# Optimization experiments

Hardware: AMD Instinct MI355X
Metric: run time of the kernel (lower is better)

Reference implementation:

```python
import jax, jax.numpy as jnp
import numpy as np

N = 100000
F_IN = 128
HID = 8
HEADS = 8
CLASSES = 40
NEG_SLOPE = 0.2


def gat_conv(x, src, dst, W, a_src, a_dst, bias, heads, out_c):
    # x: [N, F]; W: [F, heads*out_c]; a_src/a_dst: [heads, out_c]; bias: [heads*out_c]
    n = x.shape[0]
    h = (x @ W).reshape(n, heads, out_c)                       # [N, H, C]
    al_src = jnp.sum(h * a_src, axis=-1)                       # [N, H]
    al_dst = jnp.sum(h * a_dst, axis=-1)                       # [N, H]
    e = jax.nn.leaky_relu(al_src[src] + al_dst[dst], NEG_SLOPE)  # [E, H]
    # segment softmax over destination node (PyG softmax over edge_index[1])
    m = jax.ops.segment_max(e, dst, num_segments=n)            # [N, H]
    m = jnp.where(jnp.isfinite(m), m, 0.0)
    ex = jnp.exp(e - m[dst])
    denom = jax.ops.segment_sum(ex, dst, num_segments=n)       # [N, H]
    alpha = ex / denom[dst]                                    # [E, H]
    msg = h[src] * alpha[:, :, None]                           # [E, H, C]
    out = jax.ops.segment_sum(msg, dst, num_segments=n)        # [N, H, C]
    return out.reshape(n, heads * out_c) + bias


def setup_inputs() -> dict:
    key = jax.random.key(0)
    ks = jax.random.split(key, 12)
    E = 1600000
    x = jax.random.normal(ks[0], (N, F_IN), dtype=jnp.float32)
    edge_index = jax.random.randint(ks[1], (2, E), 0, N, dtype=jnp.int32)
    # layer 1: in=F_IN, out=HID, heads=HEADS, concat -> 64 channels
    s1 = 1.0 / np.sqrt(F_IN)
    W1 = jax.random.uniform(ks[2], (F_IN, HEADS * HID), jnp.float32, -s1, s1)
    a_src1 = jax.random.uniform(ks[3], (HEADS, HID), jnp.float32, -0.3, 0.3)
    a_dst1 = jax.random.uniform(ks[4], (HEADS, HID), jnp.float32, -0.3, 0.3)
    b1 = jnp.zeros((HEADS * HID,), jnp.float32)
    # layer 2: in=64, out=CLASSES, heads=1
    d2 = HEADS * HID
    s2 = 1.0 / np.sqrt(d2)
    W2 = jax.random.uniform(ks[5], (d2, CLASSES), jnp.float32, -s2, s2)
    a_src2 = jax.random.uniform(ks[6], (1, CLASSES), jnp.float32, -0.3, 0.3)
    a_dst2 = jax.random.uniform(ks[7], (1, CLASSES), jnp.float32, -0.3, 0.3)
    b2 = jnp.zeros((CLASSES,), jnp.float32)
    return {"x": x, "edge_index": edge_index, "W1": W1, "a_src1": a_src1,
            "a_dst1": a_dst1, "b1": b1, "W2": W2, "a_src2": a_src2,
            "a_dst2": a_dst2, "b2": b2}


def reference(x, edge_index, W1, a_src1, a_dst1, b1, W2, a_src2, a_dst2, b2):
    # PyG GATConv adds self-loops by default
    loops = jnp.arange(N, dtype=edge_index.dtype)
    src = jnp.concatenate([edge_index[0], loops])
    dst = jnp.concatenate([edge_index[1], loops])
    h = gat_conv(x, src, dst, W1, a_src1, a_dst1, b1, HEADS, HID)
    h = jax.nn.relu(h)  # dropout is identity in eval mode
    out = gat_conv(h, src, dst, W2, a_src2, a_dst2, b2, 1, CLASSES)
    return jax.nn.log_softmax(out, axis=1)
```

## Files before the change

### kernel.cpp

```cpp
#include <hip/hip_runtime.h>
#include <hip/hip_bf16.h>
#include <math.h>

#define FIN 128
#define HID 8
#define HEADS 8
#define C1 64
#define CLS 40
#define NSLOPE 0.2f
#define NINF (-__builtin_inff())

typedef __hip_bfloat16 bf16;
typedef int vint4 __attribute__((ext_vector_type(4)));

__device__ __forceinline__ float lrelu(float x) { return x >= 0.f ? x : NSLOPE * x; }
__device__ __forceinline__ vint4 ldnt4(const int* p) {
    return __builtin_nontemporal_load((const vint4*)p);
}

__global__ __launch_bounds__(256) void k_deg(const int* __restrict__ ei, int E,
                                             int n, int* __restrict__ deg) {
    int g = blockIdx.x & 7;
    int per8 = (n + 7) >> 3;
    int lo = g * per8, hi = min(n, lo + per8);
    int idx = (blockIdx.x >> 3) * 256 + threadIdx.x;
    int e0 = idx * 4;
    if (e0 + 3 < E) {
        vint4 dv = ldnt4(ei + E + e0);
        if (dv.x >= lo && dv.x < hi) atomicAdd(&deg[dv.x], 1);
        if (dv.y >= lo && dv.y < hi) atomicAdd(&deg[dv.y], 1);
        if (dv.z >= lo && dv.z < hi) atomicAdd(&deg[dv.z], 1);
        if (dv.w >= lo && dv.w < hi) atomicAdd(&deg[dv.w], 1);
    } else {
        int e_end = min(e0 + 4, E);
        for (int e = e0; e < e_end; ++e) {
            int dd = ei[E + e];
            if (dd >= lo && dd < hi) atomicAdd(&deg[dd], 1);
        }
    }
}

__global__ __launch_bounds__(256) void k_scan1(const int* __restrict__ deg,
    int* __restrict__ rowstart, int* __restrict__ bsum, int n) {
    __shared__ int sm[256];
    int t = threadIdx.x, i = blockIdx.x * 256 + t;
    int v = (i < n) ? deg[i] + 1 : 0;
    sm[t] = v; __syncthreads();
    int x = v;
    for (int off = 1; off < 256; off <<= 1) {
        int tv = (t >= off) ? sm[t - off] : 0;
        __syncthreads();
        x += tv; sm[t] = x; __syncthreads();
    }
    if (i < n) rowstart[i] = x - v;
    if (t == 255) bsum[blockIdx.x] = x;
}

__global__ __launch_bounds__(512) void k_scan2(int* __restrict__ bsum, int nb) {
    __shared__ int sm[512];
    int t = threadIdx.x;
    int v = (t < nb) ? bsum[t] : 0;
    sm[t] = v; __syncthreads();
    int x = v;
    for (int off = 1; off < 512; off <<= 1) {
        int tv = (t >= off) ? sm[t - off] : 0;
        __syncthreads();
        x += tv; sm[t] = x; __syncthreads();
    }
    if (t < nb) bsum[t] = x - v;
}

__global__ void k_scan3(int* __restrict__ rowstart, const int* __restrict__ bsum,
                        int n, int total) {
    int i = blockIdx.x * blockDim.x + threadIdx.x;
    if (i < n) rowstart[i] += bsum[i >> 8];
    if (i == 0) rowstart[n] = total;
}

__global__ __launch_bounds__(256) void k_scatter(const int* __restrict__ ei,
    int E, int En, int n, int* __restrict__ rowcur, int* __restrict__ csr) {
    int g = blockIdx.x & 7;
    int per8 = (n + 7) >> 3;
    int lo = g * per8, hi = min(n, lo + per8);
    int idx = (blockIdx.x >> 3) * 256 + threadIdx.x;
    int e0 = idx * 4;
    if (e0 + 3 < E) {
        vint4 dv = ldnt4(ei + E + e0);
        vint4 sv = ldnt4(ei + e0);
        if (dv.x >= lo && dv.x < hi) csr[atomicAdd(&rowcur[dv.x], 1)] = sv.x;
        if (dv.y >= lo && dv.y < hi) csr[atomicAdd(&rowcur[dv.y], 1)] = sv.y;
        if (dv.z >= lo && dv.z < hi) csr[atomicAdd(&rowcur[dv.z], 1)] = sv.z;
        if (dv.w >= lo && dv.w < hi) csr[atomicAdd(&rowcur[dv.w], 1)] = sv.w;
    } else {
        int e_end = min(e0 + 4, En);
        for (int e = e0; e < e_end; ++e) {
            int s, d;
            if (e < E) { s = ei[e]; d = ei[E + e]; } else { s = d = e - E; }
            if (d >= lo && d < hi) csr[atomicAdd(&rowcur[d], 1)] = s;
        }
    }
}

__global__ __launch_bounds__(256) void gemm1_kernel(
    const float* __restrict__ x, const float* __restrict__ W1,
    const float* __restrict__ a_src, const float* __restrict__ a_dst,
    bf16* __restrict__ h1b, float* __restrict__ alS, float* __restrict__ alD, int n) {
    __shared__ float4 Wl[FIN][C1 / 4];
    __shared__ float xs[64][FIN + 4];
    int t = threadIdx.x;
    const float4* W4 = (const float4*)W1;
    for (int i = t; i < FIN * (C1 / 4); i += 256) Wl[i / (C1 / 4)][i % (C1 / 4)] = W4[i];
    int node0 = blockIdx.x * 64;
    for (int i = t; i < 64 * (FIN / 4); i += 256) {
        int r = i / (FIN / 4), c = i % (FIN / 4);
        int nn = node0 + r;
        float4 v = {0.f, 0.f, 0.f, 0.f};
        if (nn < n) v = ((const float4*)x)[(size_t)nn * (FIN / 4) + c];
        *(float4*)&xs[r][c * 4] = v;
    }
    __syncthreads();
    int cg = t & 15, ng = t >> 4;
    int head = cg >> 1, hc = (cg & 1) * 4;
    float acc[4][4];
    #pragma unroll
    for (int i = 0; i < 4; ++i)
        for (int j = 0; j < 4; ++j) acc[i][j] = 0.f;
    #pragma unroll 2
    for (int k = 0; k < FIN; ++k) {
        float4 w = Wl[k][cg];
        #pragma unroll
        for (int i = 0; i < 4; ++i) {
            float xv = xs[ng * 4 + i][k];
            acc[i][0] += xv * w.x; acc[i][1] += xv * w.y;
            acc[i][2] += xv * w.z; acc[i][3] += xv * w.w;
        }
    }
    float a_s[4], a_d[4];
    #pragma unroll
    for (int j = 0; j < 4; ++j) {
        a_s[j] = a_src[head * HID + hc + j];
        a_d[j] = a_dst[head * HID + hc + j];
    }
    #pragma unroll
    for (int i = 0; i < 4; ++i) {
        int node = node0 + ng * 4 + i;
        float as = acc[i][0] * a_s[0] + acc[i][1] * a_s[1]
                 + acc[i][2] * a_s[2] + acc[i][3] * a_s[3];
        float ad = acc[i][0] * a_d[0] + acc[i][1] * a_d[1]
                 + acc[i][2] * a_d[2] + acc[i][3] * a_d[3];
        as += __shfl_xor(as, 1, 64);
        ad += __shfl_xor(ad, 1, 64);
        if (node < n) {
            union { ushort4 u; bf16 b[4]; } pk;
            #pragma unroll
            for (int j = 0; j < 4; ++j) pk.b[j] = __float2bfloat16(acc[i][j]);
            ((ushort4*)h1b)[(size_t)node * (C1 / 4) + cg] = pk.u;
            if ((cg & 1) == 0) {
                alS[node * HEADS + head] = as;
                alD[node * HEADS + head] = ad;
            }
        }
    }
}

__global__ __launch_bounds__(256) void k_agg1(
    const int* __restrict__ csr, const int* __restrict__ rowend,
    const int* __restrict__ deg,
    const float* __restrict__ alS, const float* __restrict__ alD,
    const bf16* __restrict__ h1b, const float* __restrict__ b1,
    const float* __restrict__ W2, const float* __restrict__ aS2,
    const float* __restrict__ aD2,
    bf16* __restrict__ h2b, float* __restrict__ alS2, float* __restrict__ alD2,
    int n) {
    __shared__ int    ls[4][64];
    __shared__ float4 lp4[4][128];
    __shared__ float  xrow[4][64];
    __shared__ float  Wl[C1][CLS];
    int t = threadIdx.x;
    for (int i = t; i < C1 * CLS; i += 256) Wl[i / CLS][i % CLS] = W2[i];
    __syncthreads();
    int lane = t & 63, wv = t >> 6;
    int d = blockIdx.x * 4 + wv;
    if (d >= n) return;
    float4 ad0 = *(const float4*)(alD + d * HEADS);
    float4 ad1 = *(const float4*)(alD + d * HEADS + 4);
    float adh[8] = {ad0.x, ad0.y, ad0.z, ad0.w, ad1.x, ad1.y, ad1.z, ad1.w};
    int cnt  = deg[d] + 1;
    int base = rowend[d] - cnt;
    int hsel = lane >> 3;
    float acc = 0.f, den = 0.f;
    const float* lpf = (const float*)&lp4[wv][0];
    for (int jb = 0; jb < cnt; jb += 64) {
        int ec = min(64, cnt - jb);
        int jj = jb + lane;
        bool on = jj < cnt;
        int s = on ? csr[base + jj] : 0;
        ls[wv][lane] = s;
        float4 a0 = *(const float4*)(alS + s * HEADS);
        float4 a1 = *(const float4*)(alS + s * HEADS + 4);
        float av[8] = {a0.x, a0.y, a0.z, a0.w, a1.x, a1.y, a1.z, a1.w};
        float pv[8];
        #pragma unroll
        for (int h = 0; h < 8; ++h)
            pv[h] = on ? __expf(lrelu(av[h] + adh[h])) : 0.f;
        lp4[wv][lane * 2]     = make_float4(pv[0], pv[1], pv[2], pv[3]);
        lp4[wv][lane * 2 + 1] = make_float4(pv[4], pv[5], pv[6], pv[7]);
        int j = 0;
        for (; j + 4 <= ec; j += 4) {
            int s0 = ls[wv][j],     s1 = ls[wv][j + 1];
            int s2 = ls[wv][j + 2], s3 = ls[wv][j + 3];
            float p0 = lpf[(j    ) * 8 + hsel], p1 = lpf[(j + 1) * 8 + hsel];
            float p2 = lpf[(j + 2) * 8 + hsel], p3 = lpf[(j + 3) * 8 + hsel];
            float v0 = __bfloat162float(h1b[s0 * C1 + lane]);
            float v1 = __bfloat162float(h1b[s1 * C1 + lane]);
            float v2 = __bfloat162float(h1b[s2 * C1 + lane]);
            float v3 = __bfloat162float(h1b[s3 * C1 + lane]);
            acc = fmaf(p0, v0, acc); acc = fmaf(p1, v1, acc);
            acc = fmaf(p2, v2, acc); acc = fmaf(p3, v3, acc);
            den += p0 + p1 + p2 + p3;
        }
        for (; j < ec; ++j) {
            int s0 = ls[wv][j];
            float p0 = lpf[j * 8 + hsel];
            acc = fmaf(p0, __bfloat162float(h1b[s0 * C1 + lane]), acc);
            den += p0;
        }
    }
    float v = acc / den + b1[lane];
    v = v > 0.f ? v : 0.f;
    xrow[wv][lane] = v;
    bool act = lane < CLS;
    float h2c = 0.f;
    if (act) {
        #pragma unroll 8
        for (int k = 0; k < C1; ++k) h2c = fmaf(xrow[wv][k], Wl[k][lane], h2c);
    }
    float as2 = act ? h2c * aS2[lane] : 0.f;
    float ad2 = act ? h2c * aD2[lane] : 0.f;
    #pragma unroll
    for (int off = 1; off < 64; off <<= 1) {
        as2 += __shfl_xor(as2, off, 64);
        ad2 += __shfl_xor(ad2, off, 64);
    }
    if (act) h2b[d * CLS + lane] = __float2bfloat16(h2c);
    if (lane == 0) { alS2[d] = as2; alD2[d] = ad2; }
}

__global__ __launch_bounds__(256) void k_agg2(
    const int* __restrict__ csr, const int* __restrict__ rowend,
    const int* __restrict__ deg,
    const float* __restrict__ alS, const float* __restrict__ alD,
    const bf16* __restrict__ h2b, const float* __restrict__ b2,
    float* __restrict__ out, int n) {
    __shared__ int2 lsp[4][64];
    int lane = threadIdx.x & 63, wv = threadIdx.x >> 6;
    int d = blockIdx.x * 4 + wv;
    if (d >= n) return;
    float ad = alD[d];
    int cnt  = deg[d] + 1;
    int base = rowend[d] - cnt;
    bool act = lane < CLS;
    float acc = 0.f, den = 0.f;
    for (int jb = 0; jb < cnt; jb += 64) {
        int ec = min(64, cnt - jb);
        int jj = jb + lane;
        bool on = jj < cnt;
        int s = on ? csr[base + jj] : 0;
        float p = on ? __expf(lrelu(alS[s] + ad)) : 0.f;
        den += p;
        lsp[wv][lane] = make_int2(s, __float_as_int(p));
        if (act) {
            int j = 0;
            for (; j + 4 <= ec; j += 4) {
                int2 e0 = lsp[wv][j],     e1 = lsp[wv][j + 1];
                int2 e2 = lsp[wv][j + 2], e3 = lsp[wv][j + 3];
                float v0 = __bfloat162float(h2b[e0.x * CLS + lane]);
                float v1 = __bfloat162float(h2b[e1.x * CLS + lane]);
                float v2 = __bfloat162float(h2b[e2.x * CLS + lane]);
                float v3 = __bfloat162float(h2b[e3.x * CLS + lane]);
                acc = fmaf(__int_as_float(e0.y), v0, acc);
                acc = fmaf(__int_as_float(e1.y), v1, acc);
                acc = fmaf(__int_as_float(e2.y), v2, acc);
                acc = fmaf(__int_as_float(e3.y), v3, acc);
            }
            for (; j < ec; ++j) {
                int2 e0 = lsp[wv][j];
                acc = fmaf(__int_as_float(e0.y),
                           __bfloat162float(h2b[e0.x * CLS + lane]), acc);
            }
        }
    }
    #pragma unroll
    for (int off = 1; off < 64; off <<= 1) den += __shfl_xor(den, off, 64);
    float v = act ? (acc / den + b2[lane]) : NINF;
    float mx = v;
    #pragma unroll
    for (int off = 1; off < 64; off <<= 1) mx = fmaxf(mx, __shfl_xor(mx, off, 64));
    float ev = act ? __expf(v - mx) : 0.f;
    float sum = ev;
    #pragma unroll
    for (int off = 1; off < 64; off <<= 1) sum += __shfl_xor(sum, off, 64);
    float lse = mx + __logf(sum);
    if (act) out[d * CLS + lane] = v - lse;
}

extern "C" void kernel_launch(void* const* d_in, const int* in_sizes, int n_in,
                              void* d_out, int out_size, void* d_ws, size_t ws_size,
                              hipStream_t stream) {
    const float* x   = (const float*)d_in[0];
    const int*   ei  = (const int*)d_in[1];
    const float* W1  = (const float*)d_in[2];
    const float* aS1 = (const float*)d_in[3];
    const float* aD1 = (const float*)d_in[4];
    const float* b1  = (const float*)d_in[5];
    const float* W2  = (const float*)d_in[6];
    const float* aS2 = (const float*)d_in[7];
    const float* aD2 = (const float*)d_in[8];
    const float* b2  = (const float*)d_in[9];
    float* out = (float*)d_out;

    int n = in_sizes[0] / FIN;
    int E = in_sizes[1] / 2;
    int En = E + n;

    char* wsb = (char*)d_ws;
    bf16*  h1b  = (bf16*)wsb;
    bf16*  h2b  = h1b + (size_t)n * C1;
    float* alS1 = (float*)(h2b + (size_t)n * CLS);
    float* alD1 = alS1 + (size_t)n * HEADS;
    float* alS2 = alD1 + (size_t)n * HEADS;
    float* alD2 = alS2 + n;
    int*   csr  = (int*)(alD2 + n);
    int*   rowstart = csr + En;
    int*   deg  = rowstart + n + 1;
    int*   bsum = deg + n;

    const int T = 256;
    int nb = (n + 255) / 256;

    (void)hipMemsetAsync(deg, 0, (size_t)n * sizeof(int), stream);
    int chunksD = (E / 4 + T - 1) / T;
    k_deg<<<chunksD * 8, T, 0, stream>>>(ei, E, n, deg);
    k_scan1<<<nb, T, 0, stream>>>(deg, rowstart, bsum, n);
    k_scan2<<<1, 512, 0, stream>>>(bsum, nb);
    k_scan3<<<nb, T, 0, stream>>>(rowstart, bsum, n, En);
    int chunks = (En + 1023) / 1024;
    k_scatter<<<chunks * 8, T, 0, stream>>>(ei, E, En, n, rowstart, csr);

    gemm1_kernel<<<(n + 63) / 64, T, 0, stream>>>(x, W1, aS1, aD1, h1b, alS1, alD1, n);
    k_agg1<<<(n + 3) / 4, T, 0, stream>>>(csr, rowstart, deg, alS1, alD1, h1b, b1,
                                          W2, aS2, aD2, h2b, alS2, alD2, n);

    k_agg2<<<(n + 3) / 4, T, 0, stream>>>(csr, rowstart, deg, alS2, alD2, h2b, b2, out, n);
}
```

Measured before the change: 389.8 us.

## Vectorize bf16 gathers as pairs, split edges across half-waves, persistent agg1 grid

Both aggregation kernels now load two bf16 channels per 32-bit word and split each wave into two half-waves that take alternating edges. The partial sums are combined with a cross-half shuffle. k_agg1 becomes a grid-stride persistent kernel with 2048 blocks, so the 10KB W2 shared-memory staging happens once per block instead of once per 4 nodes. k_deg drops its 8-way destination-range partitioning and issues every atomic from a single pass. The aim is to cut gather instruction count and redundant W2 loads, at the risk of more atomic contention in the degree count.

```diff
diff --git a/kernel.cpp b/kernel.cpp
--- a/kernel.cpp
+++ b/kernel.cpp
@@ -11,32 +11,26 @@
 #define NINF (-__builtin_inff())
 
 typedef __hip_bfloat16 bf16;
+typedef unsigned int uint32;
 typedef int vint4 __attribute__((ext_vector_type(4)));
 
 __device__ __forceinline__ float lrelu(float x) { return x >= 0.f ? x : NSLOPE * x; }
 __device__ __forceinline__ vint4 ldnt4(const int* p) {
     return __builtin_nontemporal_load((const vint4*)p);
 }
-
-__global__ __launch_bounds__(256) void k_deg(const int* __restrict__ ei, int E,
-                                             int n, int* __restrict__ deg) {
-    int g = blockIdx.x & 7;
-    int per8 = (n + 7) >> 3;
-    int lo = g * per8, hi = min(n, lo + per8);
-    int idx = (blockIdx.x >> 3) * 256 + threadIdx.x;
+__device__ __forceinline__ float bfLO(uint32 u) { return __uint_as_float(u << 16); }
+__device__ __forceinline__ float bfHI(uint32 u) { return __uint_as_float(u & 0xffff0000u); }
+
+__global__ void k_deg(const int* __restrict__ ei, int E, int* __restrict__ deg) {
+    int idx = blockIdx.x * blockDim.x + threadIdx.x;
     int e0 = idx * 4;
     if (e0 + 3 < E) {
         vint4 dv = ldnt4(ei + E + e0);
-        if (dv.x >= lo && dv.x < hi) atomicAdd(&deg[dv.x], 1);
-        if (dv.y >= lo && dv.y < hi) atomicAdd(&deg[dv.y], 1);
-        if (dv.z >= lo && dv.z < hi) atomicAdd(&deg[dv.z], 1);
-        if (dv.w >= lo && dv.w < hi) atomicAdd(&deg[dv.w], 1);
+        atomicAdd(&deg[dv.x], 1); atomicAdd(&deg[dv.y], 1);
+        atomicAdd(&deg[dv.z], 1); atomicAdd(&deg[dv.w], 1);
     } else {
         int e_end = min(e0 + 4, E);
-        for (int e = e0; e < e_end; ++e) {
-            int dd = ei[E + e];
-            if (dd >= lo && dd < hi) atomicAdd(&deg[dd], 1);
-        }
+        for (int e = e0; e < e_end; ++e) atomicAdd(&deg[ei[E + e]], 1);
     }
 }
 
@@ -180,70 +174,87 @@
     for (int i = t; i < C1 * CLS; i += 256) Wl[i / CLS][i % CLS] = W2[i];
     __syncthreads();
     int lane = t & 63, wv = t >> 6;
-    int d = blockIdx.x * 4 + wv;
-    if (d >= n) return;
-    float4 ad0 = *(const float4*)(alD + d * HEADS);
-    float4 ad1 = *(const float4*)(alD + d * HEADS + 4);
-    float adh[8] = {ad0.x, ad0.y, ad0.z, ad0.w, ad1.x, ad1.y, ad1.z, ad1.w};
-    int cnt  = deg[d] + 1;
-    int base = rowend[d] - cnt;
-    int hsel = lane >> 3;
-    float acc = 0.f, den = 0.f;
+    int c32 = lane & 31;
+    int par = lane >> 5;
+    int hp  = c32 >> 2;
     const float* lpf = (const float*)&lp4[wv][0];
-    for (int jb = 0; jb < cnt; jb += 64) {
-        int ec = min(64, cnt - jb);
-        int jj = jb + lane;
-        bool on = jj < cnt;
-        int s = on ? csr[base + jj] : 0;
-        ls[wv][lane] = s;
-        float4 a0 = *(const float4*)(alS + s * HEADS);
-        float4 a1 = *(const float4*)(alS + s * HEADS + 4);
-        float av[8] = {a0.x, a0.y, a0.z, a0.w, a1.x, a1.y, a1.z, a1.w};
-        float pv[8];
+    const uint32* h1u = (const uint32*)h1b;
+    int stride = gridDim.x * 4;
+
+    for (int d = blockIdx.x * 4 + wv; d < n; d += stride) {
+        float4 ad0 = *(const float4*)(alD + d * HEADS);
+        float4 ad1 = *(const float4*)(alD + d * HEADS + 4);
+        float adh[8] = {ad0.x, ad0.y, ad0.z, ad0.w, ad1.x, ad1.y, ad1.z, ad1.w};
+        int cnt  = deg[d] + 1;
+        int base = rowend[d] - cnt;
+        float accx = 0.f, accy = 0.f, den = 0.f;
+        for (int jb = 0; jb < cnt; jb += 64) {
+            int ec = min(64, cnt - jb);
+            int jj = jb + lane;
+            bool on = jj < cnt;
+            int s = on ? csr[base + jj] : 0;
+            ls[wv][lane] = s;
+            float4 a0 = *(const float4*)(alS + s * HEADS);
+            float4 a1 = *(const float4*)(alS + s * HEADS + 4);
+            float av[8] = {a0.x, a0.y, a0.z, a0.w, a1.x, a1.y, a1.z, a1.w};
+            float pv[8];
+            #pragma unroll
+            for (int h = 0; h < 8; ++h)
+                pv[h] = on ? __expf(lrelu(av[h] + adh[h])) : 0.f;
+            lp4[wv][lane * 2]     = make_float4(pv[0], pv[1], pv[2], pv[3]);
+            lp4[wv][lane * 2 + 1] = make_float4(pv[4], pv[5], pv[6], pv[7]);
+            int j = 0;
+            for (; j + 8 <= ec; j += 8) {
+                int j0 = j + par, j1 = j + 2 + par, j2 = j + 4 + par, j3 = j + 6 + par;
+                int s0 = ls[wv][j0], s1 = ls[wv][j1];
+                int s2 = ls[wv][j2], s3 = ls[wv][j3];
+                float p0 = lpf[j0 * 8 + hp], p1 = lpf[j1 * 8 + hp];
+                float p2 = lpf[j2 * 8 + hp], p3 = lpf[j3 * 8 + hp];
+                uint32 u0 = h1u[s0 * 32 + c32], u1 = h1u[s1 * 32 + c32];
+                uint32 u2 = h1u[s2 * 32 + c32], u3 = h1u[s3 * 32 + c32];
+                accx = fmaf(p0, bfLO(u0), accx); accy = fmaf(p0, bfHI(u0), accy);
+                accx = fmaf(p1, bfLO(u1), accx); accy = fmaf(p1, bfHI(u1), accy);
+                accx = fmaf(p2, bfLO(u2), accx); accy = fmaf(p2, bfHI(u2), accy);
+                accx = fmaf(p3, bfLO(u3), accx); accy = fmaf(p3, bfHI(u3), accy);
+                den += p0 + p1 + p2 + p3;
+            }
+            for (; j < ec; j += 2) {
+                int j0 = j + par;
+                int s0 = ls[wv][j0];
+                float p0 = lpf[j0 * 8 + hp];
+                uint32 u0 = h1u[s0 * 32 + c32];
+                accx = fmaf(p0, bfLO(u0), accx);
+                accy = fmaf(p0, bfHI(u0), accy);
+                den += p0;
+            }
+        }
+        accx += __shfl_xor(accx, 32, 64);
+        accy += __shfl_xor(accy, 32, 64);
+        den  += __shfl_xor(den, 32, 64);
+        if (lane < 32) {
+            float2 bb = *(const float2*)(b1 + 2 * c32);
+            float vx = accx / den + bb.x;
+            float vy = accy / den + bb.y;
+            vx = vx > 0.f ? vx : 0.f;
+            vy = vy > 0.f ? vy : 0.f;
+            *(float2*)&xrow[wv][2 * c32] = make_float2(vx, vy);
+        }
+        bool act = lane < CLS;
+        float h2c = 0.f;
+        if (act) {
+            #pragma unroll 8
+            for (int k = 0; k < C1; ++k) h2c = fmaf(xrow[wv][k], Wl[k][lane], h2c);
+        }
+        float as2 = act ? h2c * aS2[lane] : 0.f;
+        float ad2 = act ? h2c * aD2[lane] : 0.f;
         #pragma unroll
-        for (int h = 0; h < 8; ++h)
-            pv[h] = on ? __expf(lrelu(av[h] + adh[h])) : 0.f;
-        lp4[wv][lane * 2]     = make_float4(pv[0], pv[1], pv[2], pv[3]);
-        lp4[wv][lane * 2 + 1] = make_float4(pv[4], pv[5], pv[6], pv[7]);
-        int j = 0;
-        for (; j + 4 <= ec; j += 4) {
-            int s0 = ls[wv][j],     s1 = ls[wv][j + 1];
-            int s2 = ls[wv][j + 2], s3 = ls[wv][j + 3];
-            float p0 = lpf[(j    ) * 8 + hsel], p1 = lpf[(j + 1) * 8 + hsel];
-            float p2 = lpf[(j + 2) * 8 + hsel], p3 = lpf[(j + 3) * 8 + hsel];
-            float v0 = __bfloat162float(h1b[s0 * C1 + lane]);
-            float v1 = __bfloat162float(h1b[s1 * C1 + lane]);
-            float v2 = __bfloat162float(h1b[s2 * C1 + lane]);
-            float v3 = __bfloat162float(h1b[s3 * C1 + lane]);
-            acc = fmaf(p0, v0, acc); acc = fmaf(p1, v1, acc);
-            acc = fmaf(p2, v2, acc); acc = fmaf(p3, v3, acc);
-            den += p0 + p1 + p2 + p3;
-        }
-        for (; j < ec; ++j) {
-            int s0 = ls[wv][j];
-            float p0 = lpf[j * 8 + hsel];
-            acc = fmaf(p0, __bfloat162float(h1b[s0 * C1 + lane]), acc);
-            den += p0;
-        }
-    }
-    float v = acc / den + b1[lane];
-    v = v > 0.f ? v : 0.f;
-    xrow[wv][lane] = v;
-    bool act = lane < CLS;
-    float h2c = 0.f;
-    if (act) {
-        #pragma unroll 8
-        for (int k = 0; k < C1; ++k) h2c = fmaf(xrow[wv][k], Wl[k][lane], h2c);
-    }
-    float as2 = act ? h2c * aS2[lane] : 0.f;
-    float ad2 = act ? h2c * aD2[lane] : 0.f;
-    #pragma unroll
-    for (int off = 1; off < 64; off <<= 1) {
-        as2 += __shfl_xor(as2, off, 64);
-        ad2 += __shfl_xor(ad2, off, 64);
-    }
-    if (act) h2b[d * CLS + lane] = __float2bfloat16(h2c);
-    if (lane == 0) { alS2[d] = as2; alD2[d] = ad2; }
+        for (int off = 1; off < 64; off <<= 1) {
+            as2 += __shfl_xor(as2, off, 64);
+            ad2 += __shfl_xor(ad2, off, 64);
+        }
+        if (act) h2b[d * CLS + lane] = __float2bfloat16(h2c);
+        if (lane == 0) { alS2[d] = as2; alD2[d] = ad2; }
+    }
 }
 
 __global__ __launch_bounds__(256) void k_agg2(
@@ -256,11 +267,14 @@
     int lane = threadIdx.x & 63, wv = threadIdx.x >> 6;
     int d = blockIdx.x * 4 + wv;
     if (d >= n) return;
+    int c32 = lane & 31;
+    int par = lane >> 5;
+    bool actB = c32 < (CLS / 2);
+    const uint32* h2u = (const uint32*)h2b;
     float ad = alD[d];
     int cnt  = deg[d] + 1;
     int base = rowend[d] - cnt;
-    bool act = lane < CLS;
-    float acc = 0.f, den = 0.f;
+    float accx = 0.f, accy = 0.f, den = 0.f;
     for (int jb = 0; jb < cnt; jb += 64) {
         int ec = min(64, cnt - jb);
         int jj = jb + lane;
@@ -269,39 +283,49 @@
         float p = on ? __expf(lrelu(alS[s] + ad)) : 0.f;
         den += p;
         lsp[wv][lane] = make_int2(s, __float_as_int(p));
-        if (act) {
+        if (actB) {
             int j = 0;
-            for (; j + 4 <= ec; j += 4) {
-                int2 e0 = lsp[wv][j],     e1 = lsp[wv][j + 1];
-                int2 e2 = lsp[wv][j + 2], e3 = lsp[wv][j + 3];
-                float v0 = __bfloat162float(h2b[e0.x * CLS + lane]);
-                float v1 = __bfloat162float(h2b[e1.x * CLS + lane]);
-                float v2 = __bfloat162float(h2b[e2.x * CLS + lane]);
-                float v3 = __bfloat162float(h2b[e3.x * CLS + lane]);
-                acc = fmaf(__int_as_float(e0.y), v0, acc);
-                acc = fmaf(__int_as_float(e1.y), v1, acc);
-                acc = fmaf(__int_as_float(e2.y), v2, acc);
-                acc = fmaf(__int_as_float(e3.y), v3, acc);
-            }
-            for (; j < ec; ++j) {
-                int2 e0 = lsp[wv][j];
-                acc = fmaf(__int_as_float(e0.y),
-                           __bfloat162float(h2b[e0.x * CLS + lane]), acc);
+            for (; j + 8 <= ec; j += 8) {
+                int2 e0 = lsp[wv][j + par],     e1 = lsp[wv][j + 2 + par];
+                int2 e2 = lsp[wv][j + 4 + par], e3 = lsp[wv][j + 6 + par];
+                uint32 u0 = h2u[e0.x * 20 + c32], u1 = h2u[e1.x * 20 + c32];
+                uint32 u2 = h2u[e2.x * 20 + c32], u3 = h2u[e3.x * 20 + c32];
+                float p0 = __int_as_float(e0.y), p1 = __int_as_float(e1.y);
+                float p2 = __int_as_float(e2.y), p3 = __int_as_float(e3.y);
+                accx = fmaf(p0, bfLO(u0), accx); accy = fmaf(p0, bfHI(u0), accy);
+                accx = fmaf(p1, bfLO(u1), accx); accy = fmaf(p1, bfHI(u1), accy);
+                accx = fmaf(p2, bfLO(u2), accx); accy = fmaf(p2, bfHI(u2), accy);
+                accx = fmaf(p3, bfLO(u3), accx); accy = fmaf(p3, bfHI(u3), accy);
+            }
+            for (; j < ec; j += 2) {
+                int2 e0 = lsp[wv][j + par];
+                uint32 u0 = h2u[e0.x * 20 + c32];
+                float p0 = __int_as_float(e0.y);
+                accx = fmaf(p0, bfLO(u0), accx);
+                accy = fmaf(p0, bfHI(u0), accy);
             }
         }
     }
     #pragma unroll
     for (int off = 1; off < 64; off <<= 1) den += __shfl_xor(den, off, 64);
-    float v = act ? (acc / den + b2[lane]) : NINF;
-    float mx = v;
+    accx += __shfl_xor(accx, 32, 64);
+    accy += __shfl_xor(accy, 32, 64);
+    bool owner = (lane < 32) && actB;
+    float vx = 0.f, vy = 0.f;
+    if (owner) {
+        float2 bb = *(const float2*)(b2 + 2 * c32);
+        vx = accx / den + bb.x;
+        vy = accy / den + bb.y;
+    }
+    float mx = owner ? fmaxf(vx, vy) : NINF;
     #pragma unroll
     for (int off = 1; off < 64; off <<= 1) mx = fmaxf(mx, __shfl_xor(mx, off, 64));
-    float ev = act ? __expf(v - mx) : 0.f;
-    float sum = ev;
+    float sum = owner ? (__expf(vx - mx) + __expf(vy - mx)) : 0.f;
     #pragma unroll
     for (int off = 1; off < 64; off <<= 1) sum += __shfl_xor(sum, off, 64);
     float lse = mx + __logf(sum);
-    if (act) out[d * CLS + lane] = v - lse;
+    if (owner)
+        *(float2*)(out + (size_t)d * CLS + 2 * c32) = make_float2(vx - lse, vy - lse);
 }
 
 extern "C" void kernel_launch(void* const* d_in, const int* in_sizes, int n_in,
@@ -339,8 +363,7 @@
     int nb = (n + 255) / 256;
 
     (void)hipMemsetAsync(deg, 0, (size_t)n * sizeof(int), stream);
-    int chunksD = (E / 4 + T - 1) / T;
-    k_deg<<<chunksD * 8, T, 0, stream>>>(ei, E, n, deg);
+    k_deg<<<(E / 4 + T - 1) / T, T, 0, stream>>>(ei, E, deg);
     k_scan1<<<nb, T, 0, stream>>>(deg, rowstart, bsum, n);
     k_scan2<<<1, 512, 0, stream>>>(bsum, nb);
     k_scan3<<<nb, T, 0, stream>>>(rowstart, bsum, n, En);
@@ -348,8 +371,8 @@
     k_scatter<<<chunks * 8, T, 0, stream>>>(ei, E, En, n, rowstart, csr);
 
     gemm1_kernel<<<(n + 63) / 64, T, 0, stream>>>(x, W1, aS1, aD1, h1b, alS1, alD1, n);
-    k_agg1<<<(n + 3) / 4, T, 0, stream>>>(csr, rowstart, deg, alS1, alD1, h1b, b1,
-                                          W2, aS2, aD2, h2b, alS2, alD2, n);
+    k_agg1<<<2048, T, 0, stream>>>(csr, rowstart, deg, alS1, alD1, h1b, b1,
+                                   W2, aS2, aD2, h2b, alS2, alD2, n);
 
     k_agg2<<<(n + 3) / 4, T, 0, stream>>>(csr, rowstart, deg, alS2, alD2, h2b, b2, out, n);
 }
```

Result: faster. 344.3 us (-11.7%).
